# Kernel optimization log

Hardware: AMD Instinct MI355X
Metric: run time of the kernel (lower is better)

Reference implementation:

```python
import jax, jax.numpy as jnp
import numpy as np

D_MODEL = 1024
N_HEADS = 16
D_KEYS = 64
GROUP_POSITIONS = [list(range(g * 32, (g + 1) * 32)) for g in range(4)]


def _make_tables(group_positions, dim):
    # InGroup table: pe[j,i] = (j/Lg) * L0 / 10000^(2*(i//2)/dim)
    L0 = len(group_positions[0])
    rows = []
    for grp in group_positions:
        Lg = len(grp)
        for j in range(Lg):
            rows.append([j / Lg * L0 / np.power(10000.0, 2 * (i // 2) / dim) for i in range(dim)])
    pe = np.array(rows)
    ingroup = np.concatenate([np.sin(pe[:, 0::2]), np.cos(pe[:, 1::2])], axis=1).astype(np.float32)
    # Sequence (group) table: pe[j,i] = grp[0] / 10000^(j/Lg), constant over i
    rows = []
    for grp in group_positions:
        Lg = len(grp)
        for j in range(Lg):
            rows.append([grp[0] / np.power(10000.0, j / Lg) for _ in range(dim)])
    pe = np.array(rows)
    seq = np.concatenate([np.sin(pe[:, 0::2]), np.cos(pe[:, 1::2])], axis=1).astype(np.float32)
    return jnp.asarray(ingroup), jnp.asarray(seq)


def setup_inputs() -> dict:
    key = jax.random.key(0)
    ks = jax.random.split(key, 12)
    B, L, S = 64, 128, 128
    dqk = D_KEYS * N_HEADS
    sc_in = 1.0 / np.sqrt(D_MODEL)
    sc_out = 1.0 / np.sqrt(dqk)
    inp = {
        "queries": jax.random.normal(ks[0], (B, L, D_MODEL), jnp.float32),
        "keys": jax.random.normal(ks[1], (B, S, D_MODEL), jnp.float32),
        "values": jax.random.normal(ks[2], (B, S, D_MODEL), jnp.float32),
        "attn_mask": jnp.zeros((B, 1, L, S), dtype=bool),
        "Wq": jax.random.normal(ks[3], (D_MODEL, dqk), jnp.float32) * sc_in,
        "bq": jnp.zeros((dqk,), jnp.float32),
        "Wk": jax.random.normal(ks[4], (D_MODEL, dqk), jnp.float32) * sc_in,
        "bk": jnp.zeros((dqk,), jnp.float32),
        "Wv": jax.random.normal(ks[5], (D_MODEL, dqk), jnp.float32) * sc_in,
        "bv": jnp.zeros((dqk,), jnp.float32),
        "Wo": jax.random.normal(ks[6], (dqk, D_MODEL), jnp.float32) * sc_out,
        "bo": jnp.zeros((D_MODEL,), jnp.float32),
    }
    pos_ingroup, pos_seq = _make_tables(GROUP_POSITIONS, D_KEYS)
    inp["pos_ingroup"] = pos_ingroup  # [n_pos, d_keys]
    inp["pos_seq"] = pos_seq          # [n_pos, d_keys]
    return inp


def _rope(x, pos):
    # x: [B, H, L, D]; pos: [L, D]
    sin, cos = jnp.split(pos, 2, axis=-1)
    sin_pos = jnp.stack([sin, sin], axis=-1).reshape(pos.shape)
    cos_pos = jnp.stack([cos, cos], axis=-1).reshape(pos.shape)
    rot = jnp.stack([-x[..., 1::2], x[..., ::2]], axis=-1).reshape(x.shape)
    return x * cos_pos + rot * sin_pos


def reference(queries, keys, values, attn_mask, Wq, bq, Wk, bk, Wv, bv, Wo, bo, pos_ingroup, pos_seq):
    B, L, _ = queries.shape
    S = keys.shape[1]
    H, E = N_HEADS, D_KEYS
    q = (queries @ Wq + bq).reshape(B, L, H, E).transpose(0, 2, 1, 3)  # [B,H,L,E]
    k = (keys @ Wk + bk).reshape(B, S, H, E).transpose(0, 2, 1, 3)
    v = (values @ Wv + bv).reshape(B, S, H, E).transpose(0, 2, 1, 3)
    # group-sequence in-group RoPE, then group RoPE (tables gathered at arange positions)
    q = _rope(_rope(q, pos_ingroup[:L]), pos_seq[:L])
    k = _rope(_rope(k, pos_ingroup[:S]), pos_seq[:S])
    # inner full attention on [B,L,H,E] layout
    scale = 1.0 / jnp.sqrt(jnp.asarray(E, q.dtype))
    scores = jnp.einsum("bhle,bhse->bhls", q, k) * scale
    scores = jnp.where(attn_mask, jnp.asarray(-jnp.inf, scores.dtype), scores)
    attn = jax.nn.softmax(scores, axis=-1)  # [B,H,L,S]
    out = jnp.einsum("bhls,bhsd->blhd", attn, v).reshape(B, L, H * E)
    return out @ Wo + bo, attn
```

## Files before the change

### kernel.cpp

```cpp
#include <hip/hip_runtime.h>
#include <cstdint>

typedef float f32x4 __attribute__((ext_vector_type(4)));
typedef __bf16 bf16x8 __attribute__((ext_vector_type(8)));

typedef __attribute__((address_space(3))) uint32_t lds_u32;
typedef __attribute__((address_space(1))) const uint32_t glb_u32;

#define GLOAD_LDS16(gp, lp) \
  __builtin_amdgcn_global_load_lds((glb_u32*)(uintptr_t)(gp), (lds_u32*)(uintptr_t)(lp), 16, 0, 0)

__device__ inline unsigned short f2bf(float f) {
  union { float f; uint32_t u; } v; v.f = f;
  uint32_t u = v.u;
  return (unsigned short)((u + 0x7fffu + ((u >> 16) & 1u)) >> 16);
}

__global__ void prep_w(const float* __restrict__ wq, const float* __restrict__ wk,
                       const float* __restrict__ wv, const float* __restrict__ wo,
                       unsigned short* __restrict__ wt)
{
  __shared__ float t[64][65];
  const int z = blockIdx.z;
  const float* W = (z == 0) ? wq : (z == 1) ? wk : (z == 2) ? wv : wo;
  unsigned short* Wt = wt + (size_t)z * 1048576;
  const int n0 = blockIdx.x * 64, k0 = blockIdx.y * 64;
  const int tx = threadIdx.x & 63, ty = threadIdx.x >> 6;
#pragma unroll
  for (int i = 0; i < 16; i++) {
    int row = i * 4 + ty;
    t[row][tx] = W[(size_t)(k0 + row) * 1024 + n0 + tx];
  }
  __syncthreads();
#pragma unroll
  for (int i = 0; i < 16; i++) {
    int row = i * 4 + ty;
    Wt[(size_t)(n0 + row) * 1024 + k0 + tx] = f2bf(t[tx][row]);
  }
}

__global__ void comb_kernel(const float* __restrict__ ing, const float* __restrict__ seq,
                            float* __restrict__ cosc, float* __restrict__ sinc)
{
  int idx = blockIdx.x * 256 + threadIdx.x;
  int j = idx >> 5, i = idx & 31;
  float s1 = ing[j * 64 + i], c1 = ing[j * 64 + 32 + i];
  float s2 = seq[j * 64 + i], c2 = seq[j * 64 + 32 + i];
  cosc[idx] = c1 * c2 - s1 * s2;
  sinc[idx] = s1 * c2 + c1 * s2;
}

__global__ void cvt_kernel(const float* __restrict__ q, const float* __restrict__ k,
                           const float* __restrict__ v, unsigned short* __restrict__ dst)
{
  const int z = blockIdx.z;
  const float* src = (z == 0) ? q : (z == 1) ? k : v;
  unsigned short* d = dst + (size_t)z * 8388608;
  size_t i = ((size_t)blockIdx.x * 256 + threadIdx.x) * 4;
  float4 f = *(const float4*)&src[i];
  ushort4 o;
  o.x = f2bf(f.x); o.y = f2bf(f.y); o.z = f2bf(f.z); o.w = f2bf(f.w);
  *(ushort4*)&d[i] = o;
}

__global__ __launch_bounds__(256, 2)
void gemm_bt(const unsigned short* __restrict__ Abase,
             const unsigned short* __restrict__ Bbase,
             const float* __restrict__ b0, const float* __restrict__ b1,
             const float* __restrict__ b2,
             unsigned short* __restrict__ qb, unsigned short* __restrict__ kb,
             unsigned short* __restrict__ vtb,
             float* __restrict__ outf,
             const float* __restrict__ cosc, const float* __restrict__ sinc,
             int final_mode)
{
  __shared__ __attribute__((aligned(16))) unsigned short As[128 * 64];
  __shared__ __attribute__((aligned(16))) unsigned short Bs[128 * 64];

  const int tid = threadIdx.x;
  const int lane = tid & 63;
  const int wave = tid >> 6;
  const int quad = lane >> 4;
  const int l15 = lane & 15;

  const int z = blockIdx.z;
  const int tileM = blockIdx.x * 128;
  const int tileN = blockIdx.y * 128;
  const int K = 1024;

  const unsigned short* A = Abase + (size_t)z * (8192u * 1024u);
  const unsigned short* B = Bbase + (size_t)z * (1024u * 1024u);

  const int wm = (wave >> 1) * 64;
  const int wn = (wave & 1) * 64;

  f32x4 acc[4][4];
#pragma unroll
  for (int a = 0; a < 4; a++)
#pragma unroll
    for (int n = 0; n < 4; n++)
      acc[a][n] = (f32x4){0.f, 0.f, 0.f, 0.f};

  for (int k0 = 0; k0 < K; k0 += 64) {
#pragma unroll
    for (int cc = 0; cc < 4; cc++) {
      int c = wave * 4 + cc;
      int s = c * 64 + lane;
      int row = s >> 3;
      int gc = (s & 7) ^ (row & 7);
      const unsigned short* ga = A + (size_t)(tileM + row) * K + k0 + gc * 8;
      const unsigned short* gb = B + (size_t)(tileN + row) * K + k0 + gc * 8;
      GLOAD_LDS16(ga, &As[c * 512]);
      GLOAD_LDS16(gb, &Bs[c * 512]);
    }
    __syncthreads();

#pragma unroll
    for (int ks = 0; ks < 2; ks++) {
      bf16x8 af[4], bfr[4];
#pragma unroll
      for (int a = 0; a < 4; a++) {
        int r = wm + a * 16 + l15;
        int cp = (ks * 4 + quad) ^ (r & 7);
        af[a] = *(const bf16x8*)&As[(r * 8 + cp) * 8];
      }
#pragma unroll
      for (int n = 0; n < 4; n++) {
        int r = wn + n * 16 + l15;
        int cp = (ks * 4 + quad) ^ (r & 7);
        bfr[n] = *(const bf16x8*)&Bs[(r * 8 + cp) * 8];
      }
#pragma unroll
      for (int a = 0; a < 4; a++)
#pragma unroll
        for (int n = 0; n < 4; n++)
          acc[a][n] = __builtin_amdgcn_mfma_f32_16x16x32_bf16(af[a], bfr[n], acc[a][n], 0, 0, 0);
    }
    __syncthreads();
  }

  if (final_mode) {
#pragma unroll
    for (int n = 0; n < 4; n++) {
      int cg = tileN + wn + n * 16 + l15;
      float bias = b0[cg];
#pragma unroll
      for (int a = 0; a < 4; a++)
#pragma unroll
        for (int reg = 0; reg < 4; reg++) {
          int r = tileM + wm + a * 16 + quad * 4 + reg;
          outf[(size_t)r * 1024 + cg] = acc[a][n][reg] + bias;
        }
    }
  } else {
    const float* bias = (z == 0) ? b0 : (z == 1) ? b1 : b2;
    unsigned short* outq = (z == 0) ? qb : kb;
#pragma unroll
    for (int n = 0; n < 4; n++) {
      int cg = tileN + wn + n * 16 + l15;
      float bv_ = bias[cg];
      int h = cg >> 6, e = cg & 63;
#pragma unroll
      for (int a = 0; a < 4; a++)
#pragma unroll
        for (int reg = 0; reg < 4; reg++) {
          int r = tileM + wm + a * 16 + quad * 4 + reg;
          int bb = r >> 7, l = r & 127;
          float v = acc[a][n][reg] + bv_;
          if (z == 2) {
            vtb[(((size_t)bb * 16 + h) * 64 + e) * 128 + l] = f2bf(v);
          } else {
            float other = __shfl_xor(v, 1);
            float cs = cosc[l * 32 + (e >> 1)];
            float sn = sinc[l * 32 + (e >> 1)];
            float res = v * cs + ((e & 1) ? other : -other) * sn;
            outq[(((size_t)bb * 16 + h) * 128 + l) * 64 + e] = f2bf(res);
          }
        }
    }
  }
}

__global__ __launch_bounds__(256, 2)
void attn_kernel(const unsigned short* __restrict__ qb,
                 const unsigned short* __restrict__ kb,
                 const unsigned short* __restrict__ vtb,
                 const unsigned char* __restrict__ mask,
                 float* __restrict__ attn_out,
                 unsigned short* __restrict__ ob)
{
  __shared__ __attribute__((aligned(16))) unsigned short Pb[128 * 136];
  const int tid = threadIdx.x;
  const int lane = tid & 63;
  const int wave = tid >> 6;
  const int quad = lane >> 4;
  const int l15 = lane & 15;
  const int bh = blockIdx.x;
  const int b = bh >> 4;
  const int h = bh & 15;

  const unsigned short* q = qb + (size_t)bh * 128 * 64;
  const unsigned short* k = kb + (size_t)bh * 128 * 64;
  const unsigned short* vt = vtb + (size_t)bh * 64 * 128;

  f32x4 sacc[2][8];
#pragma unroll
  for (int mt = 0; mt < 2; mt++)
#pragma unroll
    for (int nt = 0; nt < 8; nt++)
      sacc[mt][nt] = (f32x4){0.f, 0.f, 0.f, 0.f};

#pragma unroll
  for (int ks = 0; ks < 2; ks++) {
    bf16x8 aq[2], bk[8];
#pragma unroll
    for (int mt = 0; mt < 2; mt++)
      aq[mt] = *(const bf16x8*)&q[(size_t)(wave * 32 + mt * 16 + l15) * 64 + ks * 32 + quad * 8];
#pragma unroll
    for (int nt = 0; nt < 8; nt++)
      bk[nt] = *(const bf16x8*)&k[(size_t)(nt * 16 + l15) * 64 + ks * 32 + quad * 8];
#pragma unroll
    for (int mt = 0; mt < 2; mt++)
#pragma unroll
      for (int nt = 0; nt < 8; nt++)
        sacc[mt][nt] = __builtin_amdgcn_mfma_f32_16x16x32_bf16(aq[mt], bk[nt], sacc[mt][nt], 0, 0, 0);
  }

  const float scale = 0.125f;
#pragma unroll
  for (int mt = 0; mt < 2; mt++) {
#pragma unroll
    for (int reg = 0; reg < 4; reg++) {
      int r = wave * 32 + mt * 16 + quad * 4 + reg;
      const unsigned char* mrow = mask + ((size_t)b * 128 + r) * 128;
      float sv[8];
#pragma unroll
      for (int nt = 0; nt < 8; nt++) {
        float x = sacc[mt][nt][reg] * scale;
        if (mrow[nt * 16 + l15]) x = -__builtin_inff();
        sv[nt] = x;
      }
      float m = sv[0];
#pragma unroll
      for (int nt = 1; nt < 8; nt++) m = fmaxf(m, sv[nt]);
#pragma unroll
      for (int off = 1; off < 16; off <<= 1) m = fmaxf(m, __shfl_xor(m, off));
      float s = 0.f;
#pragma unroll
      for (int nt = 0; nt < 8; nt++) { sv[nt] = __expf(sv[nt] - m); s += sv[nt]; }
#pragma unroll
      for (int off = 1; off < 16; off <<= 1) s += __shfl_xor(s, off);
      float inv = 1.0f / s;
      float* arow = attn_out + ((size_t)bh * 128 + r) * 128;
#pragma unroll
      for (int nt = 0; nt < 8; nt++) {
        float p = sv[nt] * inv;
        arow[nt * 16 + l15] = p;
        Pb[r * 136 + nt * 16 + l15] = f2bf(p);
      }
    }
  }
  __syncthreads();

  f32x4 oacc[2][4];
#pragma unroll
  for (int mt = 0; mt < 2; mt++)
#pragma unroll
    for (int nt = 0; nt < 4; nt++)
      oacc[mt][nt] = (f32x4){0.f, 0.f, 0.f, 0.f};

#pragma unroll
  for (int ks = 0; ks < 4; ks++) {
    bf16x8 bv[4], ap[2];
#pragma unroll
    for (int nt = 0; nt < 4; nt++)
      bv[nt] = *(const bf16x8*)&vt[(size_t)(nt * 16 + l15) * 128 + ks * 32 + quad * 8];
#pragma unroll
    for (int mt = 0; mt < 2; mt++)
      ap[mt] = *(const bf16x8*)&Pb[(size_t)(wave * 32 + mt * 16 + l15) * 136 + ks * 32 + quad * 8];
#pragma unroll
    for (int mt = 0; mt < 2; mt++)
#pragma unroll
      for (int nt = 0; nt < 4; nt++)
        oacc[mt][nt] = __builtin_amdgcn_mfma_f32_16x16x32_bf16(ap[mt], bv[nt], oacc[mt][nt], 0, 0, 0);
  }

#pragma unroll
  for (int mt = 0; mt < 2; mt++)
#pragma unroll
    for (int nt = 0; nt < 4; nt++)
#pragma unroll
      for (int reg = 0; reg < 4; reg++) {
        int r = wave * 32 + mt * 16 + quad * 4 + reg;
        int e = nt * 16 + l15;
        ob[((size_t)b * 128 + r) * 1024 + h * 64 + e] = f2bf(oacc[mt][nt][reg]);
      }
}

extern "C" void kernel_launch(void* const* d_in, const int* in_sizes, int n_in,
                              void* d_out, int out_size, void* d_ws, size_t ws_size,
                              hipStream_t stream)
{
  const float* queries = (const float*)d_in[0];
  const float* keys    = (const float*)d_in[1];
  const float* values  = (const float*)d_in[2];
  const unsigned char* mask = (const unsigned char*)d_in[3];
  const float* Wq = (const float*)d_in[4];
  const float* bq = (const float*)d_in[5];
  const float* Wk = (const float*)d_in[6];
  const float* bk = (const float*)d_in[7];
  const float* Wv = (const float*)d_in[8];
  const float* bv = (const float*)d_in[9];
  const float* Wo = (const float*)d_in[10];
  const float* bo = (const float*)d_in[11];
  const float* ping = (const float*)d_in[12];
  const float* pseq = (const float*)d_in[13];

  float* out  = (float*)d_out;
  float* attn = out + 8388608;
  unsigned short* Xbf = (unsigned short*)attn;

  char* ws = (char*)d_ws;
  unsigned short* Wt  = (unsigned short*)(ws);
  float* cosc = (float*)(ws + 8388608);
  float* sinc = (float*)(ws + 8388608 + 16384);
  unsigned short* qbuf = (unsigned short*)(ws + 8421376);
  unsigned short* kbuf = (unsigned short*)(ws + 8421376 + 16777216);
  unsigned short* vtbuf= (unsigned short*)(ws + 8421376 + 2*16777216);
  unsigned short* obuf = (unsigned short*)(ws + 8421376 + 3*16777216);

  prep_w<<<dim3(16, 16, 4), 256, 0, stream>>>(Wq, Wk, Wv, Wo, Wt);
  comb_kernel<<<16, 256, 0, stream>>>(ping, pseq, cosc, sinc);
  cvt_kernel<<<dim3(8192, 1, 3), 256, 0, stream>>>(queries, keys, values, Xbf);
  gemm_bt<<<dim3(64, 8, 3), 256, 0, stream>>>(Xbf, Wt, bq, bk, bv,
                                              qbuf, kbuf, vtbuf, nullptr,
                                              cosc, sinc, 0);
  attn_kernel<<<dim3(1024), 256, 0, stream>>>(qbuf, kbuf, vtbuf, mask, attn, obuf);
  gemm_bt<<<dim3(64, 8, 1), 256, 0, stream>>>(obuf, Wt + 3 * 1048576, bo, bo, bo,
                                              qbuf, kbuf, vtbuf, out,
                                              cosc, sinc, 1);
}
```

Baseline: 345.7 us.

## Add 256x256-tile double-buffered QKV projection GEMM with 8 waves

Replaces the 128x128-tile QKV projection GEMM with a new kernel using 256x256 tiles, 512 threads, and double-buffered LDS with direct global-to-LDS loads interleaved between MFMA phases. Larger tiles raise arithmetic intensity and cut global traffic per FLOP, and the staged loads are meant to overlap memory with compute. The grid drops to 384 blocks and LDS use reaches 128KB per block, which may limit occupancy and leave CUs unevenly loaded. The bias, RoPE and V-transpose epilogue is carried over.

```diff
diff --git a/kernel.cpp b/kernel.cpp
--- a/kernel.cpp
+++ b/kernel.cpp
@@ -61,6 +61,182 @@
   ushort4 o;
   o.x = f2bf(f.x); o.y = f2bf(f.y); o.z = f2bf(f.z); o.w = f2bf(f.w);
   *(ushort4*)&d[i] = o;
+}
+
+__global__ __launch_bounds__(512, 2)
+void gemm256(const unsigned short* __restrict__ Abase,
+             const unsigned short* __restrict__ Bbase,
+             const float* __restrict__ b0, const float* __restrict__ b1,
+             const float* __restrict__ b2,
+             unsigned short* __restrict__ qb, unsigned short* __restrict__ kb,
+             unsigned short* __restrict__ vtb,
+             const float* __restrict__ cosc, const float* __restrict__ sinc)
+{
+  __shared__ __attribute__((aligned(16))) unsigned short lds[2][2][16384];
+
+  const int tid = threadIdx.x;
+  const int lane = tid & 63;
+  const int wave = tid >> 6;
+  const int quad = lane >> 4;
+  const int l15 = lane & 15;
+
+  const int z = blockIdx.z;
+  const int tileM = blockIdx.x * 256;
+  const int tileN = blockIdx.y * 256;
+
+  const unsigned short* A = Abase + (size_t)z * (8192u * 1024u);
+  const unsigned short* B = Bbase + (size_t)z * (1024u * 1024u);
+
+  const int wm = (wave >> 2) * 128;
+  const int wn = (wave & 3) * 64;
+
+  int oA[8], oB[4];
+#pragma unroll
+  for (int a = 0; a < 8; a++) oA[a] = (wm + a * 16 + l15) * 64;
+#pragma unroll
+  for (int n = 0; n < 4; n++) oB[n] = (wn + n * 16 + l15) * 64;
+  const int cp0 = (quad ^ (l15 & 7)) * 8;
+  const int cp1 = ((4 + quad) ^ (l15 & 7)) * 8;
+
+  const unsigned short* sA[2][2];
+  const unsigned short* sB[2][2];
+#pragma unroll
+  for (int h = 0; h < 2; h++)
+#pragma unroll
+    for (int j = 0; j < 2; j++) {
+      int g = tid + j * 512;
+      int lr = g >> 3;
+      int gc = (g & 7) ^ (lr & 7);
+      sA[h][j] = A + (size_t)(tileM + h * 128 + lr) * 1024 + gc * 8;
+      sB[h][j] = B + (size_t)(tileN + h * 128 + lr) * 1024 + gc * 8;
+    }
+
+  auto stageA = [&](int buf, int kn) {
+#pragma unroll
+    for (int h = 0; h < 2; h++)
+#pragma unroll
+      for (int j = 0; j < 2; j++)
+        GLOAD_LDS16(sA[h][j] + kn, &lds[buf][0][h * 8192 + (wave * 64 + j * 512) * 8]);
+  };
+  auto stageB = [&](int buf, int kn) {
+#pragma unroll
+    for (int h = 0; h < 2; h++)
+#pragma unroll
+      for (int j = 0; j < 2; j++)
+        GLOAD_LDS16(sB[h][j] + kn, &lds[buf][1][h * 8192 + (wave * 64 + j * 512) * 8]);
+  };
+
+  f32x4 acc[8][4];
+#pragma unroll
+  for (int a = 0; a < 8; a++)
+#pragma unroll
+    for (int n = 0; n < 4; n++)
+      acc[a][n] = (f32x4){0.f, 0.f, 0.f, 0.f};
+
+  stageA(0, 0);
+  stageB(0, 0);
+  asm volatile("s_waitcnt vmcnt(0)" ::: "memory");
+  __builtin_amdgcn_sched_barrier(0);
+  __builtin_amdgcn_s_barrier();
+
+  for (int t = 0; t < 16; ++t) {
+    const int cur = t & 1;
+    const int nxt = cur ^ 1;
+    const unsigned short* As_ = &lds[cur][0][0];
+    const unsigned short* Bs_ = &lds[cur][1][0];
+    const int kn = (t + 1) * 64;
+    bf16x8 af[4], bfr[4];
+
+#pragma unroll
+    for (int i = 0; i < 4; i++) af[i] = *(const bf16x8*)&As_[oA[i] + cp0];
+#pragma unroll
+    for (int n = 0; n < 4; n++) bfr[n] = *(const bf16x8*)&Bs_[oB[n] + cp0];
+    if (t < 15) stageA(nxt, kn);
+    __builtin_amdgcn_s_barrier();
+    asm volatile("s_waitcnt lgkmcnt(0)" ::: "memory");
+    __builtin_amdgcn_sched_barrier(0);
+    __builtin_amdgcn_s_setprio(1);
+#pragma unroll
+    for (int i = 0; i < 4; i++)
+#pragma unroll
+      for (int n = 0; n < 4; n++)
+        acc[i][n] = __builtin_amdgcn_mfma_f32_16x16x32_bf16(af[i], bfr[n], acc[i][n], 0, 0, 0);
+    __builtin_amdgcn_s_setprio(0);
+    __builtin_amdgcn_s_barrier();
+
+#pragma unroll
+    for (int i = 0; i < 4; i++) af[i] = *(const bf16x8*)&As_[oA[4 + i] + cp0];
+    if (t < 15) stageB(nxt, kn);
+    __builtin_amdgcn_s_barrier();
+    asm volatile("s_waitcnt lgkmcnt(0)" ::: "memory");
+    __builtin_amdgcn_sched_barrier(0);
+    __builtin_amdgcn_s_setprio(1);
+#pragma unroll
+    for (int i = 0; i < 4; i++)
+#pragma unroll
+      for (int n = 0; n < 4; n++)
+        acc[4 + i][n] = __builtin_amdgcn_mfma_f32_16x16x32_bf16(af[i], bfr[n], acc[4 + i][n], 0, 0, 0);
+    __builtin_amdgcn_s_setprio(0);
+    __builtin_amdgcn_s_barrier();
+
+#pragma unroll
+    for (int i = 0; i < 4; i++) af[i] = *(const bf16x8*)&As_[oA[i] + cp1];
+#pragma unroll
+    for (int n = 0; n < 4; n++) bfr[n] = *(const bf16x8*)&Bs_[oB[n] + cp1];
+    __builtin_amdgcn_s_barrier();
+    asm volatile("s_waitcnt lgkmcnt(0)" ::: "memory");
+    __builtin_amdgcn_sched_barrier(0);
+    __builtin_amdgcn_s_setprio(1);
+#pragma unroll
+    for (int i = 0; i < 4; i++)
+#pragma unroll
+      for (int n = 0; n < 4; n++)
+        acc[i][n] = __builtin_amdgcn_mfma_f32_16x16x32_bf16(af[i], bfr[n], acc[i][n], 0, 0, 0);
+    __builtin_amdgcn_s_setprio(0);
+    __builtin_amdgcn_s_barrier();
+
+#pragma unroll
+    for (int i = 0; i < 4; i++) af[i] = *(const bf16x8*)&As_[oA[4 + i] + cp1];
+    __builtin_amdgcn_s_barrier();
+    asm volatile("s_waitcnt lgkmcnt(0)" ::: "memory");
+    __builtin_amdgcn_sched_barrier(0);
+    __builtin_amdgcn_s_setprio(1);
+#pragma unroll
+    for (int i = 0; i < 4; i++)
+#pragma unroll
+      for (int n = 0; n < 4; n++)
+        acc[4 + i][n] = __builtin_amdgcn_mfma_f32_16x16x32_bf16(af[i], bfr[n], acc[4 + i][n], 0, 0, 0);
+    __builtin_amdgcn_s_setprio(0);
+    asm volatile("s_waitcnt vmcnt(0)" ::: "memory");
+    __builtin_amdgcn_sched_barrier(0);
+    __builtin_amdgcn_s_barrier();
+  }
+
+  const float* bias = (z == 0) ? b0 : (z == 1) ? b1 : b2;
+  unsigned short* outq = (z == 0) ? qb : kb;
+#pragma unroll
+  for (int n = 0; n < 4; n++) {
+    int cg = tileN + wn + n * 16 + l15;
+    float bv_ = bias[cg];
+    int h = cg >> 6, e = cg & 63;
+#pragma unroll
+    for (int a = 0; a < 8; a++)
+#pragma unroll
+      for (int reg = 0; reg < 4; reg++) {
+        int r = tileM + wm + a * 16 + quad * 4 + reg;
+        int bb = r >> 7, l = r & 127;
+        float v = acc[a][n][reg] + bv_;
+        if (z == 2) {
+          vtb[(((size_t)bb * 16 + h) * 64 + e) * 128 + l] = f2bf(v);
+        } else {
+          float other = __shfl_xor(v, 1);
+          float cs = cosc[l * 32 + (e >> 1)];
+          float sn = sinc[l * 32 + (e >> 1)];
+          float res = v * cs + ((e & 1) ? other : -other) * sn;
+          outq[(((size_t)bb * 16 + h) * 128 + l) * 64 + e] = f2bf(res);
+        }
+      }
+  }
 }
 
 __global__ __launch_bounds__(256, 2)
@@ -332,9 +508,8 @@
   prep_w<<<dim3(16, 16, 4), 256, 0, stream>>>(Wq, Wk, Wv, Wo, Wt);
   comb_kernel<<<16, 256, 0, stream>>>(ping, pseq, cosc, sinc);
   cvt_kernel<<<dim3(8192, 1, 3), 256, 0, stream>>>(queries, keys, values, Xbf);
-  gemm_bt<<<dim3(64, 8, 3), 256, 0, stream>>>(Xbf, Wt, bq, bk, bv,
-                                              qbuf, kbuf, vtbuf, nullptr,
-                                              cosc, sinc, 0);
+  gemm256<<<dim3(32, 4, 3), 512, 0, stream>>>(Xbf, Wt, bq, bk, bv,
+                                              qbuf, kbuf, vtbuf, cosc, sinc);
   attn_kernel<<<dim3(1024), 256, 0, stream>>>(qbuf, kbuf, vtbuf, mask, attn, obuf);
   gemm_bt<<<dim3(64, 8, 1), 256, 0, stream>>>(obuf, Wt + 3 * 1048576, bo, bo, bo,
                                               qbuf, kbuf, vtbuf, out,
```

Result: slower. 391.8 us (+13.3%).
